# Performance work log

Measured on AMD Instinct MI355X. Metric: run time of the kernel, lower is better.

The kernel has to match this reference:

```python
import jax, jax.numpy as jnp
import numpy as np

B, T, C = 8, 4096, 256
N_LAYER, LAYER_ID = 12, 5


def setup_inputs() -> dict:
    key = jax.random.key(0)
    ks = jax.random.split(key, 5)
    x = jax.random.normal(ks[0], (B, T, C), dtype=jnp.float32)
    scale = 1.0 / np.sqrt(C)
    Wk = jax.random.normal(ks[1], (C, C), jnp.float32) * scale
    Wv = jax.random.normal(ks[2], (C, C), jnp.float32) * scale
    Wr = jax.random.normal(ks[3], (C, C), jnp.float32) * scale
    Wo = jax.random.normal(ks[4], (C, C), jnp.float32) * scale
    # 'fancy' init from _init_weights
    ratio_0_to_1 = LAYER_ID / (N_LAYER - 1)
    h = np.arange(C, dtype=np.float64)
    decay = -5.0 + 8.0 * (h / (C - 1)) ** (0.7 + 1.3 * ratio_0_to_1)
    zigzag = ((np.arange(C) + 1) % 3 - 1) * 0.5
    first = np.log(0.3) + zigzag
    return dict(
        x=x, Wk=Wk, Wv=Wv, Wr=Wr, Wo=Wo,
        spatial_decay=jnp.asarray(decay, jnp.float32),
        spatial_first=jnp.asarray(first, jnp.float32),
        ln_w=jnp.ones((C,), jnp.float32),
        ln_b=jnp.zeros((C,), jnp.float32),
    )


def _wkv(w, u, k, v):
    # Numerically-stable RWKV WKV scan, matching wkv_cuda forward.
    # w, u: [C] (already divided by T); k, v: [B, T, C]. Returns y: [B, T, C].
    MIN_VALUE = -1e38

    def step(carry, kv):
        p, q, o = carry            # [B, C] each
        kt, vt = kv                # [B, C]
        no = jnp.maximum(o, u + kt)
        a = jnp.exp(o - no)
        b = jnp.exp(u + kt - no)
        y = (a * p + b * vt) / (a * q + b)
        no2 = jnp.maximum(w + o, kt)
        a2 = jnp.exp(w + o - no2)
        b2 = jnp.exp(kt - no2)
        return (a2 * p + b2 * vt, a2 * q + b2, no2), y

    p0 = jnp.zeros(k.shape[0:1] + k.shape[2:3], k.dtype)  # [B, C]
    q0 = jnp.zeros_like(p0)
    o0 = jnp.full_like(p0, MIN_VALUE)
    kT = jnp.swapaxes(k, 0, 1)  # [T, B, C]
    vT = jnp.swapaxes(v, 0, 1)
    _, yT = jax.lax.scan(step, (p0, q0, o0), (kT, vT))
    return jnp.swapaxes(yT, 0, 1)


def _layernorm(x, w, b, eps=1e-5):
    mu = jnp.mean(x, axis=-1, keepdims=True)
    xc = x - mu
    var = jnp.mean(xc * xc, axis=-1, keepdims=True)
    return xc * jax.lax.rsqrt(var + eps) * w + b


def reference(x, Wk, Wv, Wr, Wo, spatial_decay, spatial_first, ln_w, ln_b):
    # shift_pixel == 0 -> xk = xv = xr = x (module's own code path)
    t = x.shape[1]
    k = jnp.einsum('btc,dc->btd', x, Wk)
    v = jnp.einsum('btc,dc->btd', x, Wv)
    r = jnp.einsum('btc,dc->btd', x, Wr)
    sr = jax.nn.sigmoid(r)
    y = _wkv(spatial_decay / t, spatial_first / t, k, v)
    y = _layernorm(y, ln_w, ln_b)
    return jnp.einsum('btc,dc->btd', sr * y, Wo)
```

## Files before the change

kernel.cpp:

```cpp
#include <hip/hip_runtime.h>
#include <cstdint>
#include <cstddef>

#define B_ 8
#define T_ 4096
#define C_ 256
#define NC_ 256
#define L_ (T_ / NC_)
#define M_ (B_ * T_)

typedef float f32x4 __attribute__((ext_vector_type(4)));
typedef short bf16x8 __attribute__((ext_vector_type(8)));

__device__ __forceinline__ unsigned short f2b(float f) {
    unsigned int u = __float_as_uint(f);
    u += 0x7fffu + ((u >> 16) & 1u);
    return (unsigned short)(u >> 16);
}
__device__ __forceinline__ float b2f(unsigned short h) {
    return __uint_as_float(((unsigned int)h) << 16);
}

__global__ __launch_bounds__(256) void cvt_w(const float* __restrict__ Wk,
                                             const float* __restrict__ Wv,
                                             const float* __restrict__ Wr,
                                             const float* __restrict__ Wo,
                                             unsigned short* __restrict__ wb) {
    const int r = blockIdx.x;
    const int mat = r >> 5;
    const float* src = (mat == 0) ? Wk : (mat == 1) ? Wv : (mat == 2) ? Wr : Wo;
    unsigned short* dst = wb + (size_t)mat * 65536;
    const size_t i = (size_t)(r & 31) * 2048 + (size_t)threadIdx.x * 8;
    float4 a = *(const float4*)(src + i);
    float4 b = *(const float4*)(src + i + 4);
    bf16x8 o;
    o[0] = (short)f2b(a.x); o[1] = (short)f2b(a.y);
    o[2] = (short)f2b(a.z); o[3] = (short)f2b(a.w);
    o[4] = (short)f2b(b.x); o[5] = (short)f2b(b.y);
    o[6] = (short)f2b(b.z); o[7] = (short)f2b(b.w);
    *(bf16x8*)(dst + i) = o;
}

__global__ __launch_bounds__(256, 3) void gemm_qkv(const float* __restrict__ x,
                                                   const unsigned short* __restrict__ w0,
                                                   const unsigned short* __restrict__ w1,
                                                   const unsigned short* __restrict__ w2,
                                                   const float* __restrict__ decay,
                                                   unsigned short* __restrict__ kb,
                                                   unsigned short* __restrict__ vb,
                                                   unsigned short* __restrict__ b2,
                                                   float* __restrict__ sp,
                                                   float* __restrict__ sq,
                                                   float* __restrict__ so) {
    __shared__ unsigned short wlds[64 * 264];
    __shared__ float stage[4][16 * 68];
    const int tid = threadIdx.x;
    const int wave = tid >> 6, lane = tid & 63;
    const int quad = lane >> 4, l16 = lane & 15;
    const int m0 = blockIdx.x * 64 + wave * 16;
    float* myst = stage[wave];

    bf16x8 af[8];
    {
        const float* Ar = x + (size_t)(m0 + l16) * C_ + quad * 8;
#pragma unroll
        for (int kc = 0; kc < 8; ++kc) {
            float4 a = *(const float4*)(Ar + kc * 32);
            float4 b = *(const float4*)(Ar + kc * 32 + 4);
            bf16x8 o;
            o[0] = (short)f2b(a.x); o[1] = (short)f2b(a.y);
            o[2] = (short)f2b(a.z); o[3] = (short)f2b(a.w);
            o[4] = (short)f2b(b.x); o[5] = (short)f2b(b.y);
            o[6] = (short)f2b(b.z); o[7] = (short)f2b(b.w);
            af[kc] = o;
        }
    }

    const int r = tid >> 5;
    const int cs = (tid & 31) * 8;
    const int bb = m0 / T_;
    const int chunk = (m0 % T_) / L_;
    const size_t colbase = ((size_t)bb * NC_ + chunk) * C_;

    bf16x8 tmp[8];
#pragma unroll
    for (int it = 0; it < 8; ++it)
        tmp[it] = *(const bf16x8*)(w0 + (size_t)(it * 8 + r) * C_ + cs);

    float kreg[16], vreg[16];

    for (int s = 0; s < 4; ++s) {
        const int n0 = s * 64;
        for (int mat = 0; mat < 3; ++mat) {
            __syncthreads();
#pragma unroll
            for (int it = 0; it < 8; ++it)
                *(bf16x8*)(wlds + (it * 8 + r) * 264 + cs) = tmp[it];
            __syncthreads();

            if (!(s == 3 && mat == 2)) {
                const unsigned short* Wn = (mat == 0) ? w1 : (mat == 1) ? w2 : w0;
                const int nn = (mat == 2) ? n0 + 64 : n0;
#pragma unroll
                for (int it = 0; it < 8; ++it)
                    tmp[it] = *(const bf16x8*)(Wn + (size_t)(nn + it * 8 + r) * C_ + cs);
            }

            f32x4 acc[4];
#pragma unroll
            for (int nt = 0; nt < 4; ++nt) acc[nt] = (f32x4){0.f, 0.f, 0.f, 0.f};
#pragma unroll
            for (int nt = 0; nt < 4; ++nt) {
                const unsigned short* wrow = wlds + (nt * 16 + l16) * 264 + quad * 8;
#pragma unroll
                for (int kc = 0; kc < 8; ++kc) {
                    bf16x8 wf = *(const bf16x8*)(wrow + kc * 32);
                    acc[nt] = __builtin_amdgcn_mfma_f32_16x16x32_bf16(af[kc], wf, acc[nt], 0, 0, 0);
                }
            }

#pragma unroll
            for (int nt = 0; nt < 4; ++nt)
#pragma unroll
                for (int i = 0; i < 4; ++i)
                    myst[(quad * 4 + i) * 68 + nt * 16 + l16] = acc[nt][i];

            const int ch = n0 + lane;
            unsigned short* dst = (mat == 0) ? kb : (mat == 1) ? vb : b2;
            unsigned short* cd = dst + (colbase + ch) * 16;
            if (mat == 0) {
                bf16x8 p0, p1;
#pragma unroll
                for (int j = 0; j < 8; ++j) p0[j] = (short)f2b(myst[j * 68 + lane]);
#pragma unroll
                for (int j = 0; j < 8; ++j) p1[j] = (short)f2b(myst[(8 + j) * 68 + lane]);
                *(bf16x8*)(cd) = p0;
                *(bf16x8*)(cd + 8) = p1;
#pragma unroll
                for (int j = 0; j < 8; ++j) {
                    kreg[j] = b2f((unsigned short)p0[j]);
                    kreg[8 + j] = b2f((unsigned short)p1[j]);
                }
            } else if (mat == 1) {
                bf16x8 p0, p1;
#pragma unroll
                for (int j = 0; j < 8; ++j) p0[j] = (short)f2b(myst[j * 68 + lane]);
#pragma unroll
                for (int j = 0; j < 8; ++j) p1[j] = (short)f2b(myst[(8 + j) * 68 + lane]);
                *(bf16x8*)(cd) = p0;
                *(bf16x8*)(cd + 8) = p1;
#pragma unroll
                for (int j = 0; j < 8; ++j) {
                    vreg[j] = b2f((unsigned short)p0[j]);
                    vreg[8 + j] = b2f((unsigned short)p1[j]);
                }
                const float w = decay[ch] * (1.0f / T_);
                float p = 0.f, q = 0.f, o = -1e38f;
#pragma unroll
                for (int j = 0; j < L_; ++j) {
                    float wo = w + o;
                    float no = fmaxf(wo, kreg[j]);
                    float a2 = __expf(wo - no), b2s = __expf(kreg[j] - no);
                    p = a2 * p + b2s * vreg[j];
                    q = a2 * q + b2s;
                    o = no;
                }
                const size_t idx = colbase + ch;
                sp[idx] = p; sq[idx] = q; so[idx] = o;
            } else {
                bf16x8 p0, p1;
#pragma unroll
                for (int j = 0; j < 8; ++j)
                    p0[j] = (short)f2b(1.f / (1.f + __expf(-myst[j * 68 + lane])));
#pragma unroll
                for (int j = 0; j < 8; ++j)
                    p1[j] = (short)f2b(1.f / (1.f + __expf(-myst[(8 + j) * 68 + lane])));
                *(bf16x8*)(cd) = p0;
                *(bf16x8*)(cd + 8) = p1;
            }
        }
    }
}

__global__ __launch_bounds__(256, 3) void gemm_out(const unsigned short* __restrict__ A,
                                                   const unsigned short* __restrict__ w0,
                                                   float* __restrict__ f0) {
    __shared__ unsigned short wlds[64 * 264];
    __shared__ float stage[4][16 * 68];
    const int tid = threadIdx.x;
    const int wave = tid >> 6, lane = tid & 63;
    const int quad = lane >> 4, l16 = lane & 15;
    const int m0 = blockIdx.x * 64 + wave * 16;
    float* myst = stage[wave];

    bf16x8 af[8];
    {
        const unsigned short* Ar = A + (size_t)(m0 + l16) * C_ + quad * 8;
#pragma unroll
        for (int kc = 0; kc < 8; ++kc) af[kc] = *(const bf16x8*)(Ar + kc * 32);
    }

    const int r = tid >> 5;
    const int cs = (tid & 31) * 8;

    bf16x8 tmp[8];
#pragma unroll
    for (int it = 0; it < 8; ++it)
        tmp[it] = *(const bf16x8*)(w0 + (size_t)(it * 8 + r) * C_ + cs);

    for (int s = 0; s < 4; ++s) {
        const int n0 = s * 64;
        __syncthreads();
#pragma unroll
        for (int it = 0; it < 8; ++it)
            *(bf16x8*)(wlds + (it * 8 + r) * 264 + cs) = tmp[it];
        __syncthreads();

        if (s < 3) {
#pragma unroll
            for (int it = 0; it < 8; ++it)
                tmp[it] = *(const bf16x8*)(w0 + (size_t)(n0 + 64 + it * 8 + r) * C_ + cs);
        }

        f32x4 acc[4];
#pragma unroll
        for (int nt = 0; nt < 4; ++nt) acc[nt] = (f32x4){0.f, 0.f, 0.f, 0.f};
#pragma unroll
        for (int nt = 0; nt < 4; ++nt) {
            const unsigned short* wrow = wlds + (nt * 16 + l16) * 264 + quad * 8;
#pragma unroll
            for (int kc = 0; kc < 8; ++kc) {
                bf16x8 wf = *(const bf16x8*)(wrow + kc * 32);
                acc[nt] = __builtin_amdgcn_mfma_f32_16x16x32_bf16(af[kc], wf, acc[nt], 0, 0, 0);
            }
        }

#pragma unroll
        for (int nt = 0; nt < 4; ++nt)
#pragma unroll
            for (int i = 0; i < 4; ++i)
                myst[(quad * 4 + i) * 68 + nt * 16 + l16] = acc[nt][i];
#pragma unroll
        for (int rr = 0; rr < 4; ++rr) {
            const int row = rr * 4 + quad;
            float4 t4 = *(const float4*)&myst[row * 68 + l16 * 4];
            *(float4*)(f0 + (size_t)(m0 + row) * C_ + n0 + l16 * 4) = t4;
        }
    }
}

__global__ __launch_bounds__(256) void wkv_combine_par(const float* __restrict__ decay,
                                                       float* __restrict__ sp,
                                                       float* __restrict__ sq,
                                                       float* __restrict__ so) {
    __shared__ float tp[16][17], tq[16][17], to[16][17];
    const int tid = threadIdx.x;
    const int cgi = tid >> 4;
    const int cl = tid & 15;
    const int b = blockIdx.x;
    const int c = blockIdx.y * 16 + cl;
    const float wL = decay[c] * (1.0f / T_) * (float)L_;
    const float wL16 = wL * 16.0f;
    const size_t base = ((size_t)b * NC_ + (size_t)cgi * 16) * C_ + c;

    float p = 0.f, q = 0.f, o = -1e38f;
#pragma unroll 4
    for (int j = 0; j < 16; ++j) {
        size_t idx = base + (size_t)j * C_;
        float lp = sp[idx], lq = sq[idx], lo = so[idx];
        float ow = o + wL;
        float no = fmaxf(ow, lo);
        float ea = __expf(ow - no), eb = __expf(lo - no);
        p = ea * p + eb * lp;
        q = ea * q + eb * lq;
        o = no;
    }
    tp[cgi][cl] = p; tq[cgi][cl] = q; to[cgi][cl] = o;

    float ip = p, iq = q, io = o;
#pragma unroll
    for (int off = 1; off < 16; off <<= 1) {
        __syncthreads();
        float ap = 0.f, aq = 0.f, ao = 0.f;
        const bool doit = (cgi >= off);
        if (doit) { ap = tp[cgi - off][cl]; aq = tq[cgi - off][cl]; ao = to[cgi - off][cl]; }
        __syncthreads();
        if (doit) {
            float ow = ao + (float)off * wL16;
            float no = fmaxf(ow, io);
            float ea = __expf(ow - no), eb = __expf(io - no);
            ip = ea * ap + eb * ip;
            iq = ea * aq + eb * iq;
            io = no;
            tp[cgi][cl] = ip; tq[cgi][cl] = iq; to[cgi][cl] = io;
        }
    }
    __syncthreads();

    float ep, eq, eo;
    if (cgi == 0) { ep = 0.f; eq = 0.f; eo = -1e38f; }
    else          { ep = tp[cgi - 1][cl]; eq = tq[cgi - 1][cl]; eo = to[cgi - 1][cl]; }

    for (int j = 0; j < 16; ++j) {
        size_t idx = base + (size_t)j * C_;
        float lp = sp[idx], lq = sq[idx], lo = so[idx];
        sp[idx] = ep; sq[idx] = eq; so[idx] = eo;
        float ow = eo + wL;
        float no = fmaxf(ow, lo);
        float ea = __expf(ow - no), eb = __expf(lo - no);
        ep = ea * ep + eb * lp;
        eq = ea * eq + eb * lq;
        eo = no;
    }
}

__global__ __launch_bounds__(256, 8) void wkv_pass2_ln(const unsigned short* __restrict__ k,
                                                       const unsigned short* __restrict__ v,
                                                       const unsigned short* __restrict__ sr,
                                                       const float* __restrict__ decay,
                                                       const float* __restrict__ first,
                                                       const float* __restrict__ lw,
                                                       const float* __restrict__ lb,
                                                       const float* __restrict__ sp,
                                                       const float* __restrict__ sq,
                                                       const float* __restrict__ so,
                                                       unsigned short* __restrict__ z) {
    __shared__ float tile[16][264];
    __shared__ float mu_s[16], rs_s[16];
    const int c = threadIdx.x, chunk = blockIdx.x, b = blockIdx.y;
    const int wave = c >> 6, lane = c & 63;
    const float w = decay[c] * (1.0f / T_);
    const float u = first[c] * (1.0f / T_);
    const float gw = lw[c], gb = lb[c];
    size_t sidx = ((size_t)b * NC_ + chunk) * C_ + c;
    float p = sp[sidx], q = sq[sidx], o = so[sidx];
    size_t base = ((size_t)b * T_ + (size_t)chunk * L_) * C_ + c;

    const unsigned short* kp = k + sidx * 16;
    const unsigned short* vp = v + sidx * 16;
    bf16x8 k0 = *(const bf16x8*)(kp), k1 = *(const bf16x8*)(kp + 8);
    bf16x8 v0 = *(const bf16x8*)(vp), v1 = *(const bf16x8*)(vp + 8);

#pragma unroll
    for (int j = 0; j < L_; ++j) {
        float kj = b2f((unsigned short)((j < 8) ? k0[j] : k1[j - 8]));
        float vj = b2f((unsigned short)((j < 8) ? v0[j] : v1[j - 8]));
        float uk = u + kj;
        float no = fmaxf(o, uk);
        float a = __expf(o - no), bb = __expf(uk - no);
        tile[j][c] = (a * p + bb * vj) / (a * q + bb);
        float wo = w + o;
        float no2 = fmaxf(wo, kj);
        float a2 = __expf(wo - no2), b2 = __expf(kj - no2);
        p = a2 * p + b2 * vj;
        q = a2 * q + b2;
        o = no2;
    }
    __syncthreads();
#pragma unroll
    for (int r = 0; r < 4; ++r) {
        const int j = wave * 4 + r;
        float4 t4 = *(const float4*)&tile[j][lane * 4];
        float s = t4.x + t4.y + t4.z + t4.w;
        float ss = t4.x * t4.x + t4.y * t4.y + t4.z * t4.z + t4.w * t4.w;
#pragma unroll
        for (int m = 1; m < 64; m <<= 1) {
            s += __shfl_xor(s, m, 64);
            ss += __shfl_xor(ss, m, 64);
        }
        if (lane == 0) {
            float mu = s * (1.f / C_);
            mu_s[j] = mu;
            rs_s[j] = rsqrtf(ss * (1.f / C_) - mu * mu + 1e-5f);
        }
    }
    __syncthreads();
    const unsigned short* srp = sr + sidx * 16;
    bf16x8 s0 = *(const bf16x8*)(srp), s1 = *(const bf16x8*)(srp + 8);
#pragma unroll
    for (int j = 0; j < L_; ++j) {
        float zz = (tile[j][c] - mu_s[j]) * rs_s[j] * gw + gb;
        zz *= b2f((unsigned short)((j < 8) ? s0[j] : s1[j - 8]));
        z[base + (size_t)j * C_] = f2b(zz);
    }
}

extern "C" void kernel_launch(void* const* d_in, const int* in_sizes, int n_in,
                              void* d_out, int out_size, void* d_ws, size_t ws_size,
                              hipStream_t stream) {
    const float* x     = (const float*)d_in[0];
    const float* Wk    = (const float*)d_in[1];
    const float* Wv    = (const float*)d_in[2];
    const float* Wr    = (const float*)d_in[3];
    const float* Wo    = (const float*)d_in[4];
    const float* decay = (const float*)d_in[5];
    const float* first = (const float*)d_in[6];
    const float* lnw   = (const float*)d_in[7];
    const float* lnb   = (const float*)d_in[8];
    float* out = (float*)d_out;

    char* ws = (char*)d_ws;
    const size_t NE = (size_t)M_ * C_;
    unsigned short* wb  = (unsigned short*)ws; ws += 4 * 65536 * 2;
    unsigned short* kbuf = (unsigned short*)ws; ws += NE * 2;
    unsigned short* vbuf = (unsigned short*)ws; ws += NE * 2;
    unsigned short* srb = (unsigned short*)ws; ws += NE * 2;
    unsigned short* zb  = (unsigned short*)ws; ws += NE * 2;
    const size_t SE = (size_t)B_ * NC_ * C_;
    float* sp = (float*)ws; ws += SE * 4;
    float* sq = (float*)ws; ws += SE * 4;
    float* so = (float*)ws; ws += SE * 4;
    unsigned short* wkb = wb;
    unsigned short* wvb = wb + 65536;
    unsigned short* wrb = wb + 2 * 65536;
    unsigned short* wob = wb + 3 * 65536;

    cvt_w<<<128, 256, 0, stream>>>(Wk, Wv, Wr, Wo, wb);

    gemm_qkv<<<dim3(M_ / 64), 256, 0, stream>>>(x, wkb, wvb, wrb, decay,
                                                kbuf, vbuf, srb, sp, sq, so);

    wkv_combine_par<<<dim3(B_, C_ / 16), 256, 0, stream>>>(decay, sp, sq, so);
    wkv_pass2_ln<<<dim3(NC_, B_), 256, 0, stream>>>(kbuf, vbuf, srb, decay, first,
                                                    lnw, lnb, sp, sq, so, zb);

    gemm_out<<<dim3(M_ / 64), 256, 0, stream>>>(zb, wob, out);
}
```

Baseline: 159.2 us.

## Split GEMM output columns across grid and read weights directly from global

Both GEMM kernels drop the LDS weight staging and its double-buffered register prefetch, loading each wave's bf16 weight fragments straight from global or L2 instead. The N dimension is now spread over a second grid axis (2 slices for the QKV GEMM, 4 for the output GEMM), so more blocks run with less serial work each, and launch_bounds no longer asks for 3 blocks per CU. The cost is that the x rows are reloaded and converted once per N-slice, and every wave re-reads the weights from cache instead of sharing them through LDS. The WKV pass also replaces a true division with a hardware reciprocal multiply, which gives slightly lower precision.

```diff
diff --git a/kernel.cpp b/kernel.cpp
--- a/kernel.cpp
+++ b/kernel.cpp
@@ -41,23 +41,23 @@
     *(bf16x8*)(dst + i) = o;
 }
 
-__global__ __launch_bounds__(256, 3) void gemm_qkv(const float* __restrict__ x,
-                                                   const unsigned short* __restrict__ w0,
-                                                   const unsigned short* __restrict__ w1,
-                                                   const unsigned short* __restrict__ w2,
-                                                   const float* __restrict__ decay,
-                                                   unsigned short* __restrict__ kb,
-                                                   unsigned short* __restrict__ vb,
-                                                   unsigned short* __restrict__ b2,
-                                                   float* __restrict__ sp,
-                                                   float* __restrict__ sq,
-                                                   float* __restrict__ so) {
-    __shared__ unsigned short wlds[64 * 264];
+__global__ __launch_bounds__(256) void gemm_qkv(const float* __restrict__ x,
+                                                const unsigned short* __restrict__ w0,
+                                                const unsigned short* __restrict__ w1,
+                                                const unsigned short* __restrict__ w2,
+                                                const float* __restrict__ decay,
+                                                unsigned short* __restrict__ kb,
+                                                unsigned short* __restrict__ vb,
+                                                unsigned short* __restrict__ b2,
+                                                float* __restrict__ sp,
+                                                float* __restrict__ sq,
+                                                float* __restrict__ so) {
     __shared__ float stage[4][16 * 68];
     const int tid = threadIdx.x;
     const int wave = tid >> 6, lane = tid & 63;
     const int quad = lane >> 4, l16 = lane & 15;
     const int m0 = blockIdx.x * 64 + wave * 16;
+    const int s0 = blockIdx.y * 2;
     float* myst = stage[wave];
 
     bf16x8 af[8];
@@ -76,47 +76,29 @@
         }
     }
 
-    const int r = tid >> 5;
-    const int cs = (tid & 31) * 8;
     const int bb = m0 / T_;
     const int chunk = (m0 % T_) / L_;
     const size_t colbase = ((size_t)bb * NC_ + chunk) * C_;
 
-    bf16x8 tmp[8];
-#pragma unroll
-    for (int it = 0; it < 8; ++it)
-        tmp[it] = *(const bf16x8*)(w0 + (size_t)(it * 8 + r) * C_ + cs);
-
     float kreg[16], vreg[16];
 
-    for (int s = 0; s < 4; ++s) {
-        const int n0 = s * 64;
+    for (int sl = 0; sl < 2; ++sl) {
+        const int n0 = (s0 + sl) * 64;
         for (int mat = 0; mat < 3; ++mat) {
-            __syncthreads();
-#pragma unroll
-            for (int it = 0; it < 8; ++it)
-                *(bf16x8*)(wlds + (it * 8 + r) * 264 + cs) = tmp[it];
-            __syncthreads();
-
-            if (!(s == 3 && mat == 2)) {
-                const unsigned short* Wn = (mat == 0) ? w1 : (mat == 1) ? w2 : w0;
-                const int nn = (mat == 2) ? n0 + 64 : n0;
-#pragma unroll
-                for (int it = 0; it < 8; ++it)
-                    tmp[it] = *(const bf16x8*)(Wn + (size_t)(nn + it * 8 + r) * C_ + cs);
-            }
+            const unsigned short* W = (mat == 0) ? w0 : (mat == 1) ? w1 : w2;
 
             f32x4 acc[4];
 #pragma unroll
             for (int nt = 0; nt < 4; ++nt) acc[nt] = (f32x4){0.f, 0.f, 0.f, 0.f};
 #pragma unroll
             for (int nt = 0; nt < 4; ++nt) {
-                const unsigned short* wrow = wlds + (nt * 16 + l16) * 264 + quad * 8;
-#pragma unroll
-                for (int kc = 0; kc < 8; ++kc) {
-                    bf16x8 wf = *(const bf16x8*)(wrow + kc * 32);
-                    acc[nt] = __builtin_amdgcn_mfma_f32_16x16x32_bf16(af[kc], wf, acc[nt], 0, 0, 0);
-                }
+                const unsigned short* wr = W + (size_t)(n0 + nt * 16 + l16) * C_ + quad * 8;
+                bf16x8 wf[8];
+#pragma unroll
+                for (int kc = 0; kc < 8; ++kc) wf[kc] = *(const bf16x8*)(wr + kc * 32);
+#pragma unroll
+                for (int kc = 0; kc < 8; ++kc)
+                    acc[nt] = __builtin_amdgcn_mfma_f32_16x16x32_bf16(af[kc], wf[kc], acc[nt], 0, 0, 0);
             }
 
 #pragma unroll
@@ -182,15 +164,15 @@
     }
 }
 
-__global__ __launch_bounds__(256, 3) void gemm_out(const unsigned short* __restrict__ A,
-                                                   const unsigned short* __restrict__ w0,
-                                                   float* __restrict__ f0) {
-    __shared__ unsigned short wlds[64 * 264];
+__global__ __launch_bounds__(256) void gemm_out(const unsigned short* __restrict__ A,
+                                                const unsigned short* __restrict__ w0,
+                                                float* __restrict__ f0) {
     __shared__ float stage[4][16 * 68];
     const int tid = threadIdx.x;
     const int wave = tid >> 6, lane = tid & 63;
     const int quad = lane >> 4, l16 = lane & 15;
     const int m0 = blockIdx.x * 64 + wave * 16;
+    const int n0 = blockIdx.y * 64;
     float* myst = stage[wave];
 
     bf16x8 af[8];
@@ -200,52 +182,30 @@
         for (int kc = 0; kc < 8; ++kc) af[kc] = *(const bf16x8*)(Ar + kc * 32);
     }
 
-    const int r = tid >> 5;
-    const int cs = (tid & 31) * 8;
-
-    bf16x8 tmp[8];
-#pragma unroll
-    for (int it = 0; it < 8; ++it)
-        tmp[it] = *(const bf16x8*)(w0 + (size_t)(it * 8 + r) * C_ + cs);
-
-    for (int s = 0; s < 4; ++s) {
-        const int n0 = s * 64;
-        __syncthreads();
-#pragma unroll
-        for (int it = 0; it < 8; ++it)
-            *(bf16x8*)(wlds + (it * 8 + r) * 264 + cs) = tmp[it];
-        __syncthreads();
-
-        if (s < 3) {
-#pragma unroll
-            for (int it = 0; it < 8; ++it)
-                tmp[it] = *(const bf16x8*)(w0 + (size_t)(n0 + 64 + it * 8 + r) * C_ + cs);
-        }
-
-        f32x4 acc[4];
-#pragma unroll
-        for (int nt = 0; nt < 4; ++nt) acc[nt] = (f32x4){0.f, 0.f, 0.f, 0.f};
-#pragma unroll
-        for (int nt = 0; nt < 4; ++nt) {
-            const unsigned short* wrow = wlds + (nt * 16 + l16) * 264 + quad * 8;
-#pragma unroll
-            for (int kc = 0; kc < 8; ++kc) {
-                bf16x8 wf = *(const bf16x8*)(wrow + kc * 32);
-                acc[nt] = __builtin_amdgcn_mfma_f32_16x16x32_bf16(af[kc], wf, acc[nt], 0, 0, 0);
-            }
-        }
-
-#pragma unroll
-        for (int nt = 0; nt < 4; ++nt)
-#pragma unroll
-            for (int i = 0; i < 4; ++i)
-                myst[(quad * 4 + i) * 68 + nt * 16 + l16] = acc[nt][i];
-#pragma unroll
-        for (int rr = 0; rr < 4; ++rr) {
-            const int row = rr * 4 + quad;
-            float4 t4 = *(const float4*)&myst[row * 68 + l16 * 4];
-            *(float4*)(f0 + (size_t)(m0 + row) * C_ + n0 + l16 * 4) = t4;
-        }
+    f32x4 acc[4];
+#pragma unroll
+    for (int nt = 0; nt < 4; ++nt) acc[nt] = (f32x4){0.f, 0.f, 0.f, 0.f};
+#pragma unroll
+    for (int nt = 0; nt < 4; ++nt) {
+        const unsigned short* wr = w0 + (size_t)(n0 + nt * 16 + l16) * C_ + quad * 8;
+        bf16x8 wf[8];
+#pragma unroll
+        for (int kc = 0; kc < 8; ++kc) wf[kc] = *(const bf16x8*)(wr + kc * 32);
+#pragma unroll
+        for (int kc = 0; kc < 8; ++kc)
+            acc[nt] = __builtin_amdgcn_mfma_f32_16x16x32_bf16(af[kc], wf[kc], acc[nt], 0, 0, 0);
+    }
+
+#pragma unroll
+    for (int nt = 0; nt < 4; ++nt)
+#pragma unroll
+        for (int i = 0; i < 4; ++i)
+            myst[(quad * 4 + i) * 68 + nt * 16 + l16] = acc[nt][i];
+#pragma unroll
+    for (int rr = 0; rr < 4; ++rr) {
+        const int row = rr * 4 + quad;
+        float4 t4 = *(const float4*)&myst[row * 68 + l16 * 4];
+        *(float4*)(f0 + (size_t)(m0 + row) * C_ + n0 + l16 * 4) = t4;
     }
 }
 
@@ -348,7 +308,7 @@
         float uk = u + kj;
         float no = fmaxf(o, uk);
         float a = __expf(o - no), bb = __expf(uk - no);
-        tile[j][c] = (a * p + bb * vj) / (a * q + bb);
+        tile[j][c] = (a * p + bb * vj) * __builtin_amdgcn_rcpf(a * q + bb);
         float wo = w + o;
         float no2 = fmaxf(wo, kj);
         float a2 = __expf(wo - no2), b2 = __expf(kj - no2);
@@ -417,12 +377,12 @@
 
     cvt_w<<<128, 256, 0, stream>>>(Wk, Wv, Wr, Wo, wb);
 
-    gemm_qkv<<<dim3(M_ / 64), 256, 0, stream>>>(x, wkb, wvb, wrb, decay,
-                                                kbuf, vbuf, srb, sp, sq, so);
+    gemm_qkv<<<dim3(M_ / 64, 2), 256, 0, stream>>>(x, wkb, wvb, wrb, decay,
+                                                   kbuf, vbuf, srb, sp, sq, so);
 
     wkv_combine_par<<<dim3(B_, C_ / 16), 256, 0, stream>>>(decay, sp, sq, so);
     wkv_pass2_ln<<<dim3(NC_, B_), 256, 0, stream>>>(kbuf, vbuf, srb, decay, first,
                                                     lnw, lnb, sp, sq, so, zb);
 
-    gemm_out<<<dim3(M_ / 64), 256, 0, stream>>>(zb, wob, out);
-}
+    gemm_out<<<dim3(M_ / 64, 4), 256, 0, stream>>>(zb, wob, out);
+}
```

Measured after the change: 259.5 us. +63.0%, slower.
